# Kernel tuning notes

Measured on AMD Instinct MI355X. Metric: run time of the kernel, lower is better.

The kernel has to match this reference:

```python
import jax, jax.numpy as jnp
import numpy as np

T, N, D, E, L = 3, 50000, 64, 800000, 2


def setup_inputs() -> dict:
    key = jax.random.key(0)
    ks = jax.random.split(key, 12)
    glorot = lambda k, shape: jax.random.uniform(
        k, shape, jnp.float32, -1.0, 1.0) * np.sqrt(6.0 / (shape[-2] + shape[-1]))
    return {
        "x": jax.random.normal(ks[0], (N, D), jnp.float32),
        "edge_index": jax.random.randint(ks[1], (2, E), 0, N),
        "edge_type": jax.random.randint(ks[2], (E,), 0, T),
        "edge_feature": jax.random.normal(ks[3], (T, D), jnp.float32),
        # per-layer parameters stacked along leading L axis
        "theta_g": glorot(ks[4], (L, T, D)),
        "theta_hi": glorot(ks[5], (L, T, D)),
        "theta_hj": glorot(ks[6], (L, T, D)),
        "we": glorot(ks[7], (L, D, D)),
        "wr": glorot(ks[8], (L, D, D)),
    }


def _scatter_softmax(r, row, n):
    # r: [T,E], softmax over edges grouped by destination node `row`
    rT = r.T  # [E,T]
    m = jax.ops.segment_max(rT, row, num_segments=n)  # [N,T]
    e = jnp.exp(rT - m[row])
    s = jax.ops.segment_sum(e, row, num_segments=n)
    return (e / s[row]).T  # [T,E]


def _layer(x, ef, tg, thi, thj, we, wr, row, col, etype, n):
    # attention logits per edge, per type-slice
    r_g = jnp.einsum('ed,td->te', ef, tg)[:, etype]          # [T,E]
    r_hi = jnp.einsum('tnd,td->tn', x, thi)[:, row]          # [T,E]
    r_hj = jnp.einsum('tnd,td->tn', x, thj)[:, col]          # [T,E]
    r = _scatter_softmax(r_g + r_hi + r_hj, row, n)          # [T,E]
    ef_new = ef @ wr                                         # [et,D]
    v = jax.nn.sigmoid(ef_new)[etype][None] * (x @ we)[:, col]  # [T,E,D]
    out = r[..., None] * v                                   # [T,E,D]
    out = jax.ops.segment_sum(out.transpose(1, 0, 2), row, num_segments=n)
    return out.transpose(1, 0, 2), ef_new                    # [T,N,D]


def reference(x, edge_index, edge_type, edge_feature, theta_g, theta_hi, theta_hj, we, wr):
    row, col = edge_index[0], edge_index[1]
    h = jnp.broadcast_to(x[None], (T, N, D))
    ef = edge_feature
    for i in range(L):
        h_prev = h
        out, ef = _layer(h, ef, theta_g[i], theta_hi[i], theta_hj[i],
                         we[i], wr[i], row, col, edge_type, N)
        if i == L - 1:
            h = out
            break
        h = h_prev + jax.nn.relu(out)  # dropout p=0 -> identity
        ef = jax.nn.relu(ef)
    return h
```

## Files before the change

kernel.cpp:

```cpp
#include <hip/hip_runtime.h>
#include <math.h>

#define TT 3
#define NN 50000
#define DD 64
#define EE 800000
#define LL 2
#define NK3 (NN * TT)
#define NB3 ((NK3 + 255) / 256)
#define CH 96

typedef _Float16 h4 __attribute__((ext_vector_type(4)));
typedef float f4 __attribute__((ext_vector_type(4)));

__global__ void k_small(const float* __restrict__ ef0,
                        const float* __restrict__ tg,
                        const float* __restrict__ wr,
                        const float* __restrict__ we,
                        const float* __restrict__ thj,
                        float* __restrict__ rg,
                        float* __restrict__ sig,
                        _Float16* __restrict__ bf)
{
    __shared__ float ef_l[TT * DD];
    __shared__ float efn[TT * DD];
    int tid = threadIdx.x;
    for (int l = 0; l < LL; ++l)
        for (int idx = tid; idx < 80 * 64; idx += 256) {
            int c = idx >> 6, k = idx & 63;
            float v = 0.f;
            if (c < 64) v = we[l * 4096 + k * 64 + c];
            else if (c < 67) v = thj[l * 192 + (c - 64) * 64 + k];
            bf[l * 5120 + idx] = (_Float16)v;
        }
    if (tid < TT * DD) ef_l[tid] = ef0[tid];
    __syncthreads();
    for (int layer = 0; layer < LL; ++layer) {
        if (tid < TT * TT) {
            int t = tid / TT, tau = tid % TT;
            float s = 0.f;
            #pragma unroll
            for (int k = 0; k < DD; ++k)
                s += ef_l[tau * DD + k] * tg[layer * TT * DD + t * DD + k];
            rg[layer * TT * TT + tid] = s;
        }
        if (tid < TT * DD) {
            int tau = tid / DD, d = tid % DD;
            float s = 0.f;
            #pragma unroll
            for (int k = 0; k < DD; ++k)
                s += ef_l[tau * DD + k] * wr[layer * DD * DD + k * DD + d];
            efn[tid] = s;
            sig[layer * TT * DD + tid] = 1.f / (1.f + expf(-s));
        }
        __syncthreads();
        if (tid < TT * DD) ef_l[tid] = fmaxf(efn[tid], 0.f);
        __syncthreads();
    }
}

__global__ void k_count3r(const int* __restrict__ row, const int* __restrict__ et,
                          int* __restrict__ counts, unsigned* __restrict__ keyrank)
{
    int e = blockIdx.x * 256 + threadIdx.x;
    if (e < EE) {
        int key = row[e] * 3 + et[e];
        int r = atomicAdd(&counts[key], 1);
        keyrank[e] = ((unsigned)key << 14) | (unsigned)r;
    }
}

__global__ void k_bsum(const int* __restrict__ counts, int* __restrict__ bsum)
{
    __shared__ int red[256];
    int i = blockIdx.x * 256 + threadIdx.x;
    red[threadIdx.x] = (i < NK3) ? counts[i] : 0;
    __syncthreads();
    for (int off = 128; off >= 1; off >>= 1) {
        if (threadIdx.x < off) red[threadIdx.x] += red[threadIdx.x + off];
        __syncthreads();
    }
    if (threadIdx.x == 0) bsum[blockIdx.x] = red[0];
}

__global__ void k_emit2(const int* __restrict__ counts,
                        const int* __restrict__ bsum,
                        int* __restrict__ csroff)
{
    __shared__ int s[256];
    __shared__ int bpre_s;
    int b = blockIdx.x, tid = threadIdx.x;
    int pp = 0;
    for (int i = tid; i < b; i += 256) pp += bsum[i];
    s[tid] = pp;
    __syncthreads();
    for (int off = 128; off >= 1; off >>= 1) {
        if (tid < off) s[tid] += s[tid + off];
        __syncthreads();
    }
    if (tid == 0) bpre_s = s[0];
    __syncthreads();
    int bpre = bpre_s;
    int idx = b * 256 + tid;
    int c = (idx < NK3) ? counts[idx] : 0;
    s[tid] = c;
    __syncthreads();
    for (int off = 1; off < 256; off <<= 1) {
        int u = (tid >= off) ? s[tid - off] : 0;
        __syncthreads();
        s[tid] += u;
        __syncthreads();
    }
    if (idx < NK3) csroff[idx] = bpre + s[tid] - c;
    if (b == NB3 - 1 && tid == 255) csroff[NK3] = bpre + s[255];
}

__global__ void k_scatter3r(const unsigned* __restrict__ keyrank,
                            const int* __restrict__ col,
                            const int* __restrict__ csroff,
                            unsigned short* __restrict__ pk)
{
    int e = blockIdx.x * 256 + threadIdx.x;
    if (e < EE) {
        unsigned kr = keyrank[e];
        int pos = csroff[kr >> 14] + (int)(kr & 16383u);
        pk[pos] = (unsigned short)col[e];
    }
}

__global__ __launch_bounds__(256) void k_mm0(
    const float* __restrict__ x,
    const _Float16* __restrict__ Bf,
    _Float16* __restrict__ hw,
    float* __restrict__ ahj)
{
    __shared__ _Float16 Ah[64][68];
    __shared__ _Float16 Bt[80][68];
    int tid = threadIdx.x;
    long rbase = (long)blockIdx.x * 64;

    #pragma unroll
    for (int it = 0; it < 4; ++it) {
        int flat = (tid + it * 256) * 4;
        int r = flat >> 6, k = flat & 63;
        h4 hv = {};
        if (rbase + r < NN) {
            float4 v = *(const float4*)&x[(rbase + r) * 64 + k];
            hv = h4{ (_Float16)v.x, (_Float16)v.y, (_Float16)v.z, (_Float16)v.w };
        }
        *(h4*)&Ah[r][k] = hv;
    }
    for (int e4 = tid; e4 < 80 * 64 / 4; e4 += 256) {
        int idx = e4 * 4;
        *(h4*)&Bt[idx >> 6][idx & 63] = *(const h4*)&Bf[idx];
    }
    __syncthreads();

    int wid = tid >> 6, lane = tid & 63;
    int r16 = lane & 15, kq = lane >> 4;
    f4 acc[5] = {};
    #pragma unroll
    for (int ks = 0; ks < 4; ++ks) {
        int k0 = ks * 16 + kq * 4;
        h4 a = *(h4*)&Ah[wid * 16 + r16][k0];
        #pragma unroll
        for (int ct = 0; ct < 5; ++ct) {
            h4 b = *(h4*)&Bt[ct * 16 + r16][k0];
            acc[ct] = __builtin_amdgcn_mfma_f32_16x16x16f16(a, b, acc[ct], 0, 0, 0);
        }
    }
    #pragma unroll
    for (int j = 0; j < 4; ++j) {
        long g = rbase + wid * 16 + kq * 4 + j;
        if (g < NN) {
            #pragma unroll
            for (int ct = 0; ct < 4; ++ct)
                hw[g * 64 + ct * 16 + r16] = (_Float16)acc[ct][j];
            if (r16 < 3) ahj[g * 4 + r16] = acc[4][j];
        }
    }
}

__global__ __launch_bounds__(256) void k_mm1(
    const _Float16* __restrict__ h,
    const _Float16* __restrict__ Bf,
    _Float16* __restrict__ hw,
    float* __restrict__ ahj)
{
    __shared__ _Float16 Ah[64][68];
    __shared__ _Float16 Bt[80][68];
    int tid = threadIdx.x;
    long rbase = (long)blockIdx.x * 64;

    #pragma unroll
    for (int it = 0; it < 4; ++it) {
        int flat = (tid + it * 256) * 4;
        int r = flat >> 6, k = flat & 63;
        h4 hv = {};
        if (rbase + r < NK3) hv = *(const h4*)&h[(rbase + r) * 64 + k];
        *(h4*)&Ah[r][k] = hv;
    }
    for (int e4 = tid; e4 < 80 * 64 / 4; e4 += 256) {
        int idx = e4 * 4;
        *(h4*)&Bt[idx >> 6][idx & 63] = *(const h4*)&Bf[idx];
    }
    __syncthreads();

    int wid = tid >> 6, lane = tid & 63;
    int r16 = lane & 15, kq = lane >> 4;
    f4 acc[5] = {};
    #pragma unroll
    for (int ks = 0; ks < 4; ++ks) {
        int k0 = ks * 16 + kq * 4;
        h4 a = *(h4*)&Ah[wid * 16 + r16][k0];
        #pragma unroll
        for (int ct = 0; ct < 5; ++ct) {
            h4 b = *(h4*)&Bt[ct * 16 + r16][k0];
            acc[ct] = __builtin_amdgcn_mfma_f32_16x16x16f16(a, b, acc[ct], 0, 0, 0);
        }
    }
    #pragma unroll
    for (int j = 0; j < 4; ++j) {
        long g = rbase + wid * 16 + kq * 4 + j;
        if (g < NK3) {
            int t = (g >= 2L * NN) ? 2 : (g >= NN ? 1 : 0);
            long n = g - (long)t * NN;
            #pragma unroll
            for (int ct = 0; ct < 4; ++ct)
                hw[((size_t)n * 3 + t) * 64 + ct * 16 + r16] = (_Float16)acc[ct][j];
            if (r16 == t) ahj[n * 4 + t] = acc[4][j];
        }
    }
}

__global__ __launch_bounds__(256) void k_edge0(
    const int* __restrict__ off3,
    const unsigned short* __restrict__ pk,
    const float* __restrict__ rg_l,
    const float* __restrict__ sig_l,
    const float* __restrict__ ahj4,
    const _Float16* __restrict__ hw,
    const float* __restrict__ x,
    _Float16* __restrict__ outh)
{
    __shared__ uint4 ent[4][CH];
    int wid = threadIdx.x >> 6, lane = threadIdx.x & 63;
    int n = blockIdx.x * 4 + wid;
    int b3 = n * 3;
    int s0 = off3[b3], s1 = off3[b3 + 1], s2 = off3[b3 + 2], s3 = off3[b3 + 3];
    float r00 = rg_l[0], r01 = rg_l[1], r02 = rg_l[2];
    float r10 = rg_l[3], r11 = rg_l[4], r12 = rg_l[5];
    float r20 = rg_l[6], r21 = rg_l[7], r22 = rg_l[8];
    float sg0 = sig_l[lane], sg1 = sig_l[64 + lane], sg2 = sig_l[128 + lane];
    const char* hwb = (const char*)hw + (size_t)lane * 2;
    uint4* myent = ent[wid];
    float acc0 = 0.f, acc1 = 0.f, acc2 = 0.f;
    float ps0 = 0.f, ps1 = 0.f, ps2 = 0.f;

    for (int base = s0; base < s3; base += CH) {
        int cnt = s3 - base; if (cnt > CH) cnt = CH;
        for (int jj = lane; jj < cnt; jj += 64) {
            int ei = base + jj;
            int c = pk[ei];
            int tau = (ei >= s1) + (ei >= s2);
            float4 aj = *(const float4*)&ahj4[c * 4];
            float g0 = (tau == 0) ? r00 : ((tau == 1) ? r01 : r02);
            float g1 = (tau == 0) ? r10 : ((tau == 1) ? r11 : r12);
            float g2 = (tau == 0) ? r20 : ((tau == 1) ? r21 : r22);
            float p0 = __expf(g0 + aj.x);
            float p1 = __expf(g1 + aj.y);
            float p2 = __expf(g2 + aj.z);
            ps0 += p0; ps1 += p1; ps2 += p2;
            myent[jj] = make_uint4(((unsigned)c * 128u) | ((unsigned)tau << 26),
                                   __float_as_uint(p0), __float_as_uint(p1),
                                   __float_as_uint(p2));
        }
        asm volatile("s_waitcnt lgkmcnt(0)" ::: "memory");

#define AGG(J) { uint4 e = myent[J];                                           \
        unsigned ta = e.x >> 26;                                               \
        float sg = (ta == 0) ? sg0 : ((ta == 1) ? sg1 : sg2);                  \
        float sv = sg * (float)*(const _Float16*)(hwb + (e.x & 0x03FFFFFFu));  \
        acc0 = fmaf(__uint_as_float(e.y), sv, acc0);                           \
        acc1 = fmaf(__uint_as_float(e.z), sv, acc1);                           \
        acc2 = fmaf(__uint_as_float(e.w), sv, acc2); }
        int j = 0;
        for (; j + 4 <= cnt; j += 4) { AGG(j) AGG(j + 1) AGG(j + 2) AGG(j + 3) }
        for (; j < cnt; ++j) { AGG(j) }
#undef AGG
        asm volatile("s_waitcnt lgkmcnt(0)" ::: "memory");
    }
    #pragma unroll
    for (int off = 32; off >= 1; off >>= 1) {
        ps0 += __shfl_xor(ps0, off);
        ps1 += __shfl_xor(ps1, off);
        ps2 += __shfl_xor(ps2, off);
    }
    float o0 = 0.f, o1 = 0.f, o2 = 0.f;
    if (s3 > s0) { o0 = acc0 / ps0; o1 = acc1 / ps1; o2 = acc2 / ps2; }
    size_t oi = (size_t)n * 64 + lane;
    float xv = x[oi];
    outh[oi]                       = (_Float16)(xv + fmaxf(o0, 0.f));
    outh[oi + (size_t)NN * 64]     = (_Float16)(xv + fmaxf(o1, 0.f));
    outh[oi + (size_t)2 * NN * 64] = (_Float16)(xv + fmaxf(o2, 0.f));
}

__global__ __launch_bounds__(256) void k_edge1(
    const int* __restrict__ off3,
    const unsigned short* __restrict__ pk,
    const float* __restrict__ rg_l,
    const float* __restrict__ sig_l,
    const float* __restrict__ ahj4,
    const _Float16* __restrict__ hw,
    float* __restrict__ outf)
{
    __shared__ uint4 ent[4][CH];
    int wid = threadIdx.x >> 6, lane = threadIdx.x & 63;
    int n = blockIdx.x * 4 + wid;
    int b3 = n * 3;
    int s0 = off3[b3], s1 = off3[b3 + 1], s2 = off3[b3 + 2], s3 = off3[b3 + 3];
    float r00 = rg_l[0], r01 = rg_l[1], r02 = rg_l[2];
    float r10 = rg_l[3], r11 = rg_l[4], r12 = rg_l[5];
    float r20 = rg_l[6], r21 = rg_l[7], r22 = rg_l[8];
    float sg0 = sig_l[lane], sg1 = sig_l[64 + lane], sg2 = sig_l[128 + lane];
    const char* hwb = (const char*)hw + (size_t)lane * 2;
    uint4* myent = ent[wid];
    float acc0 = 0.f, acc1 = 0.f, acc2 = 0.f;
    float ps0 = 0.f, ps1 = 0.f, ps2 = 0.f;

    for (int base = s0; base < s3; base += CH) {
        int cnt = s3 - base; if (cnt > CH) cnt = CH;
        for (int jj = lane; jj < cnt; jj += 64) {
            int ei = base + jj;
            int c = pk[ei];
            int tau = (ei >= s1) + (ei >= s2);
            float4 aj = *(const float4*)&ahj4[c * 4];
            float g0 = (tau == 0) ? r00 : ((tau == 1) ? r01 : r02);
            float g1 = (tau == 0) ? r10 : ((tau == 1) ? r11 : r12);
            float g2 = (tau == 0) ? r20 : ((tau == 1) ? r21 : r22);
            float p0 = __expf(g0 + aj.x);
            float p1 = __expf(g1 + aj.y);
            float p2 = __expf(g2 + aj.z);
            ps0 += p0; ps1 += p1; ps2 += p2;
            myent[jj] = make_uint4(((unsigned)c * 384u) | ((unsigned)tau << 26),
                                   __float_as_uint(p0), __float_as_uint(p1),
                                   __float_as_uint(p2));
        }
        asm volatile("s_waitcnt lgkmcnt(0)" ::: "memory");

#define AGG(J) { uint4 e = myent[J];                                           \
        unsigned ta = e.x >> 26;                                               \
        float sg = (ta == 0) ? sg0 : ((ta == 1) ? sg1 : sg2);                  \
        const char* ptr = hwb + (e.x & 0x03FFFFFFu);                           \
        float v0 = (float)*(const _Float16*)(ptr);                             \
        float v1 = (float)*(const _Float16*)(ptr + 128);                       \
        float v2 = (float)*(const _Float16*)(ptr + 256);                       \
        acc0 = fmaf(__uint_as_float(e.y), sg * v0, acc0);                      \
        acc1 = fmaf(__uint_as_float(e.z), sg * v1, acc1);                      \
        acc2 = fmaf(__uint_as_float(e.w), sg * v2, acc2); }
        int j = 0;
        for (; j + 4 <= cnt; j += 4) { AGG(j) AGG(j + 1) AGG(j + 2) AGG(j + 3) }
        for (; j < cnt; ++j) { AGG(j) }
#undef AGG
        asm volatile("s_waitcnt lgkmcnt(0)" ::: "memory");
    }
    #pragma unroll
    for (int off = 32; off >= 1; off >>= 1) {
        ps0 += __shfl_xor(ps0, off);
        ps1 += __shfl_xor(ps1, off);
        ps2 += __shfl_xor(ps2, off);
    }
    float o0 = 0.f, o1 = 0.f, o2 = 0.f;
    if (s3 > s0) { o0 = acc0 / ps0; o1 = acc1 / ps1; o2 = acc2 / ps2; }
    size_t oi = (size_t)n * 64 + lane;
    outf[oi]                       = o0;
    outf[oi + (size_t)NN * 64]     = o1;
    outf[oi + (size_t)2 * NN * 64] = o2;
}

extern "C" void kernel_launch(void* const* d_in, const int* in_sizes, int n_in,
                              void* d_out, int out_size, void* d_ws, size_t ws_size,
                              hipStream_t stream)
{
    const float* x   = (const float*)d_in[0];
    const int*   ei  = (const int*)d_in[1];
    const int*   row = ei;
    const int*   col = ei + EE;
    const int*   et  = (const int*)d_in[2];
    const float* ef  = (const float*)d_in[3];
    const float* tg  = (const float*)d_in[4];
    const float* thj = (const float*)d_in[6];
    const float* we  = (const float*)d_in[7];
    const float* wr  = (const float*)d_in[8];
    float* out = (float*)d_out;
    _Float16* h1h = (_Float16*)d_out;

    _Float16* hw1 = (_Float16*)d_ws;
    _Float16* hw0 = hw1 + (size_t)NN * 3 * 64;
    float* ahj0 = (float*)(hw0 + (size_t)NN * 64);
    float* ahj1 = ahj0 + (size_t)NN * 4;
    float* rg   = ahj1 + (size_t)NN * 4;
    float* sig  = rg + LL * 9;
    _Float16* bfB = (_Float16*)(sig + LL * 192);
    int* counts3 = (int*)(bfB + LL * 5120);
    int* csroff3 = counts3 + NK3;
    int* bsum    = csroff3 + NK3 + 1;
    unsigned* keyrank = (unsigned*)(bsum + NB3);
    unsigned short* csrpk = (unsigned short*)(keyrank + EE);

    hipMemsetAsync(counts3, 0, NK3 * sizeof(int), stream);
    k_small<<<1, 256, 0, stream>>>(ef, tg, wr, we, thj, rg, sig, bfB);
    k_count3r<<<(EE + 255) / 256, 256, 0, stream>>>(row, et, counts3, keyrank);
    k_bsum<<<NB3, 256, 0, stream>>>(counts3, bsum);
    k_emit2<<<NB3, 256, 0, stream>>>(counts3, bsum, csroff3);
    k_scatter3r<<<(EE + 255) / 256, 256, 0, stream>>>(keyrank, col, csroff3, csrpk);

    k_mm0<<<(NN + 63) / 64, 256, 0, stream>>>(x, bfB, hw0, ahj0);
    k_edge0<<<NN / 4, 256, 0, stream>>>(csroff3, csrpk, rg, sig, ahj0, hw0,
                                        x, h1h);
    k_mm1<<<(NK3 + 63) / 64, 256, 0, stream>>>(h1h, bfB + 5120, hw1, ahj1);
    k_edge1<<<NN / 4, 256, 0, stream>>>(csroff3, csrpk, rg + 9, sig + 192,
                                        ahj1, hw1, out);
}
```

Baseline: 179.5 us.

## Fuse count, layer-0 matmul and small setup into one kernel; fuse layer-1 matmul into edge0

Merges the edge counting, the first-layer feature matmul and the tiny parameter-setup kernel into one launch that dispatches by block index, so independent work shares a grid. The layer-1 matmul is folded into the end of the layer-0 edge kernel: per-node results are staged in shared memory and multiplied with MFMA instead of being written to global memory and read back. It also adds an 8-way unroll in the layer-1 aggregation loop. In exchange, the fused matmul uses only 3 of 16 MFMA rows, each edge block must load the weight tile and sync, and the extra shared memory may lower occupancy.

```diff
diff --git a/kernel.cpp b/kernel.cpp
--- a/kernel.cpp
+++ b/kernel.cpp
@@ -9,22 +9,88 @@
 #define NK3 (NN * TT)
 #define NB3 ((NK3 + 255) / 256)
 #define CH 96
+#define NBC ((EE + 255) / 256)
+#define NBM ((NN + 63) / 64)
 
 typedef _Float16 h4 __attribute__((ext_vector_type(4)));
 typedef float f4 __attribute__((ext_vector_type(4)));
 
-__global__ void k_small(const float* __restrict__ ef0,
-                        const float* __restrict__ tg,
-                        const float* __restrict__ wr,
-                        const float* __restrict__ we,
-                        const float* __restrict__ thj,
-                        float* __restrict__ rg,
-                        float* __restrict__ sig,
-                        _Float16* __restrict__ bf)
-{
-    __shared__ float ef_l[TT * DD];
-    __shared__ float efn[TT * DD];
-    int tid = threadIdx.x;
+__global__ __launch_bounds__(256) void k_fusedA(
+    const int* __restrict__ row, const int* __restrict__ et,
+    int* __restrict__ counts, unsigned* __restrict__ keyrank,
+    const float* __restrict__ x,
+    const float* __restrict__ we,
+    const float* __restrict__ thj,
+    _Float16* __restrict__ hw0,
+    float* __restrict__ ahj0,
+    const float* __restrict__ ef0,
+    const float* __restrict__ tg,
+    const float* __restrict__ wr,
+    float* __restrict__ rg,
+    float* __restrict__ sig,
+    _Float16* __restrict__ bf)
+{
+    __shared__ _Float16 Ah[64][68];
+    __shared__ _Float16 Bt[80][68];
+    int b = blockIdx.x, tid = threadIdx.x;
+
+    if (b < NBC) {
+        int e = b * 256 + tid;
+        if (e < EE) {
+            int key = row[e] * 3 + et[e];
+            int r = atomicAdd(&counts[key], 1);
+            keyrank[e] = ((unsigned)key << 14) | (unsigned)r;
+        }
+        return;
+    }
+    if (b < NBC + NBM) {
+        long rbase = (long)(b - NBC) * 64;
+        #pragma unroll
+        for (int it = 0; it < 4; ++it) {
+            int flat = (tid + it * 256) * 4;
+            int r = flat >> 6, k = flat & 63;
+            h4 hv = {};
+            if (rbase + r < NN) {
+                float4 v = *(const float4*)&x[(rbase + r) * 64 + k];
+                hv = h4{ (_Float16)v.x, (_Float16)v.y, (_Float16)v.z, (_Float16)v.w };
+            }
+            *(h4*)&Ah[r][k] = hv;
+        }
+        for (int idx = tid; idx < 80 * 64; idx += 256) {
+            int c = idx >> 6, k = idx & 63;
+            float v = 0.f;
+            if (c < 64) v = we[k * 64 + c];
+            else if (c < 67) v = thj[(c - 64) * 64 + k];
+            Bt[c][k] = (_Float16)v;
+        }
+        __syncthreads();
+        int wid = tid >> 6, lane = tid & 63;
+        int r16 = lane & 15, kq = lane >> 4;
+        f4 acc[5] = {};
+        #pragma unroll
+        for (int ks = 0; ks < 4; ++ks) {
+            int k0 = ks * 16 + kq * 4;
+            h4 a = *(h4*)&Ah[wid * 16 + r16][k0];
+            #pragma unroll
+            for (int ct = 0; ct < 5; ++ct) {
+                h4 bb = *(h4*)&Bt[ct * 16 + r16][k0];
+                acc[ct] = __builtin_amdgcn_mfma_f32_16x16x16f16(a, bb, acc[ct], 0, 0, 0);
+            }
+        }
+        #pragma unroll
+        for (int j = 0; j < 4; ++j) {
+            long g = rbase + wid * 16 + kq * 4 + j;
+            if (g < NN) {
+                #pragma unroll
+                for (int ct = 0; ct < 4; ++ct)
+                    hw0[g * 64 + ct * 16 + r16] = (_Float16)acc[ct][j];
+                if (r16 < 3) ahj0[g * 4 + r16] = acc[4][j];
+            }
+        }
+        return;
+    }
+    float* ef_l = (float*)&Ah[0][0];
+    float* efn  = ef_l + TT * DD;
     for (int l = 0; l < LL; ++l)
         for (int idx = tid; idx < 80 * 64; idx += 256) {
             int c = idx >> 6, k = idx & 63;
@@ -59,17 +125,6 @@
     }
 }
 
-__global__ void k_count3r(const int* __restrict__ row, const int* __restrict__ et,
-                          int* __restrict__ counts, unsigned* __restrict__ keyrank)
-{
-    int e = blockIdx.x * 256 + threadIdx.x;
-    if (e < EE) {
-        int key = row[e] * 3 + et[e];
-        int r = atomicAdd(&counts[key], 1);
-        keyrank[e] = ((unsigned)key << 14) | (unsigned)r;
-    }
-}
-
 __global__ void k_bsum(const int* __restrict__ counts, int* __restrict__ bsum)
 {
     __shared__ int red[256];
@@ -128,112 +183,7 @@
     }
 }
 
-__global__ __launch_bounds__(256) void k_mm0(
-    const float* __restrict__ x,
-    const _Float16* __restrict__ Bf,
-    _Float16* __restrict__ hw,
-    float* __restrict__ ahj)
-{
-    __shared__ _Float16 Ah[64][68];
-    __shared__ _Float16 Bt[80][68];
-    int tid = threadIdx.x;
-    long rbase = (long)blockIdx.x * 64;
-
-    #pragma unroll
-    for (int it = 0; it < 4; ++it) {
-        int flat = (tid + it * 256) * 4;
-        int r = flat >> 6, k = flat & 63;
-        h4 hv = {};
-        if (rbase + r < NN) {
-            float4 v = *(const float4*)&x[(rbase + r) * 64 + k];
-            hv = h4{ (_Float16)v.x, (_Float16)v.y, (_Float16)v.z, (_Float16)v.w };
-        }
-        *(h4*)&Ah[r][k] = hv;
-    }
-    for (int e4 = tid; e4 < 80 * 64 / 4; e4 += 256) {
-        int idx = e4 * 4;
-        *(h4*)&Bt[idx >> 6][idx & 63] = *(const h4*)&Bf[idx];
-    }
-    __syncthreads();
-
-    int wid = tid >> 6, lane = tid & 63;
-    int r16 = lane & 15, kq = lane >> 4;
-    f4 acc[5] = {};
-    #pragma unroll
-    for (int ks = 0; ks < 4; ++ks) {
-        int k0 = ks * 16 + kq * 4;
-        h4 a = *(h4*)&Ah[wid * 16 + r16][k0];
-        #pragma unroll
-        for (int ct = 0; ct < 5; ++ct) {
-            h4 b = *(h4*)&Bt[ct * 16 + r16][k0];
-            acc[ct] = __builtin_amdgcn_mfma_f32_16x16x16f16(a, b, acc[ct], 0, 0, 0);
-        }
-    }
-    #pragma unroll
-    for (int j = 0; j < 4; ++j) {
-        long g = rbase + wid * 16 + kq * 4 + j;
-        if (g < NN) {
-            #pragma unroll
-            for (int ct = 0; ct < 4; ++ct)
-                hw[g * 64 + ct * 16 + r16] = (_Float16)acc[ct][j];
-            if (r16 < 3) ahj[g * 4 + r16] = acc[4][j];
-        }
-    }
-}
-
-__global__ __launch_bounds__(256) void k_mm1(
-    const _Float16* __restrict__ h,
-    const _Float16* __restrict__ Bf,
-    _Float16* __restrict__ hw,
-    float* __restrict__ ahj)
-{
-    __shared__ _Float16 Ah[64][68];
-    __shared__ _Float16 Bt[80][68];
-    int tid = threadIdx.x;
-    long rbase = (long)blockIdx.x * 64;
-
-    #pragma unroll
-    for (int it = 0; it < 4; ++it) {
-        int flat = (tid + it * 256) * 4;
-        int r = flat >> 6, k = flat & 63;
-        h4 hv = {};
-        if (rbase + r < NK3) hv = *(const h4*)&h[(rbase + r) * 64 + k];
-        *(h4*)&Ah[r][k] = hv;
-    }
-    for (int e4 = tid; e4 < 80 * 64 / 4; e4 += 256) {
-        int idx = e4 * 4;
-        *(h4*)&Bt[idx >> 6][idx & 63] = *(const h4*)&Bf[idx];
-    }
-    __syncthreads();
-
-    int wid = tid >> 6, lane = tid & 63;
-    int r16 = lane & 15, kq = lane >> 4;
-    f4 acc[5] = {};
-    #pragma unroll
-    for (int ks = 0; ks < 4; ++ks) {
-        int k0 = ks * 16 + kq * 4;
-        h4 a = *(h4*)&Ah[wid * 16 + r16][k0];
-        #pragma unroll
-        for (int ct = 0; ct < 5; ++ct) {
-            h4 b = *(h4*)&Bt[ct * 16 + r16][k0];
-            acc[ct] = __builtin_amdgcn_mfma_f32_16x16x16f16(a, b, acc[ct], 0, 0, 0);
-        }
-    }
-    #pragma unroll
-    for (int j = 0; j < 4; ++j) {
-        long g = rbase + wid * 16 + kq * 4 + j;
-        if (g < NK3) {
-            int t = (g >= 2L * NN) ? 2 : (g >= NN ? 1 : 0);
-            long n = g - (long)t * NN;
-            #pragma unroll
-            for (int ct = 0; ct < 4; ++ct)
-                hw[((size_t)n * 3 + t) * 64 + ct * 16 + r16] = (_Float16)acc[ct][j];
-            if (r16 == t) ahj[n * 4 + t] = acc[4][j];
-        }
-    }
-}
-
-__global__ __launch_bounds__(256) void k_edge0(
+__global__ __launch_bounds__(256) void k_edge0mm(
     const int* __restrict__ off3,
     const unsigned short* __restrict__ pk,
     const float* __restrict__ rg_l,
@@ -241,11 +191,21 @@
     const float* __restrict__ ahj4,
     const _Float16* __restrict__ hw,
     const float* __restrict__ x,
-    _Float16* __restrict__ outh)
+    const _Float16* __restrict__ Bf1,
+    _Float16* __restrict__ hw1,
+    float* __restrict__ ahj1)
 {
     __shared__ uint4 ent[4][CH];
-    int wid = threadIdx.x >> 6, lane = threadIdx.x & 63;
+    __shared__ _Float16 Bt[80][68];
+    __shared__ _Float16 As[4][3][68];
+    int tid = threadIdx.x, wid = tid >> 6, lane = tid & 63;
     int n = blockIdx.x * 4 + wid;
+
+    for (int e4 = tid; e4 < 80 * 64 / 4; e4 += 256) {
+        int idx = e4 * 4;
+        *(h4*)&Bt[idx >> 6][idx & 63] = *(const h4*)&Bf1[idx];
+    }
+
     int b3 = n * 3;
     int s0 = off3[b3], s1 = off3[b3 + 1], s2 = off3[b3 + 2], s3 = off3[b3 + 3];
     float r00 = rg_l[0], r01 = rg_l[1], r02 = rg_l[2];
@@ -298,11 +258,37 @@
     }
     float o0 = 0.f, o1 = 0.f, o2 = 0.f;
     if (s3 > s0) { o0 = acc0 / ps0; o1 = acc1 / ps1; o2 = acc2 / ps2; }
-    size_t oi = (size_t)n * 64 + lane;
-    float xv = x[oi];
-    outh[oi]                       = (_Float16)(xv + fmaxf(o0, 0.f));
-    outh[oi + (size_t)NN * 64]     = (_Float16)(xv + fmaxf(o1, 0.f));
-    outh[oi + (size_t)2 * NN * 64] = (_Float16)(xv + fmaxf(o2, 0.f));
+    float xv = x[(size_t)n * 64 + lane];
+    As[wid][0][lane] = (_Float16)(xv + fmaxf(o0, 0.f));
+    As[wid][1][lane] = (_Float16)(xv + fmaxf(o1, 0.f));
+    As[wid][2][lane] = (_Float16)(xv + fmaxf(o2, 0.f));
+    __syncthreads();
+
+    int r16 = lane & 15, kq = lane >> 4;
+    int ar = (r16 < 3) ? r16 : 0;
+    f4 acc[5] = {};
+    #pragma unroll
+    for (int ks = 0; ks < 4; ++ks) {
+        int k0 = ks * 16 + kq * 4;
+        h4 a = *(h4*)&As[wid][ar][k0];
+        #pragma unroll
+        for (int ct = 0; ct < 5; ++ct) {
+            h4 bb = *(h4*)&Bt[ct * 16 + r16][k0];
+            acc[ct] = __builtin_amdgcn_mfma_f32_16x16x16f16(a, bb, acc[ct], 0, 0, 0);
+        }
+    }
+    if (kq == 0) {
+        #pragma unroll
+        for (int ct = 0; ct < 4; ++ct) {
+            hw1[((size_t)n * 3 + 0) * 64 + ct * 16 + r16] = (_Float16)acc[ct][0];
+            hw1[((size_t)n * 3 + 1) * 64 + ct * 16 + r16] = (_Float16)acc[ct][1];
+            hw1[((size_t)n * 3 + 2) * 64 + ct * 16 + r16] = (_Float16)acc[ct][2];
+        }
+        if (r16 < 3) {
+            float av = (r16 == 0) ? acc[4][0] : ((r16 == 1) ? acc[4][1] : acc[4][2]);
+            ahj1[n * 4 + r16] = av;
+        }
+    }
 }
 
 __global__ __launch_bounds__(256) void k_edge1(
@@ -359,6 +345,8 @@
         acc1 = fmaf(__uint_as_float(e.z), sg * v1, acc1);                      \
         acc2 = fmaf(__uint_as_float(e.w), sg * v2, acc2); }
         int j = 0;
+        for (; j + 8 <= cnt; j += 8) { AGG(j) AGG(j + 1) AGG(j + 2) AGG(j + 3)
+                                       AGG(j + 4) AGG(j + 5) AGG(j + 6) AGG(j + 7) }
         for (; j + 4 <= cnt; j += 4) { AGG(j) AGG(j + 1) AGG(j + 2) AGG(j + 3) }
         for (; j < cnt; ++j) { AGG(j) }
 #undef AGG
@@ -393,7 +381,6 @@
     const float* we  = (const float*)d_in[7];
     const float* wr  = (const float*)d_in[8];
     float* out = (float*)d_out;
-    _Float16* h1h = (_Float16*)d_out;
 
     _Float16* hw1 = (_Float16*)d_ws;
     _Float16* hw0 = hw1 + (size_t)NN * 3 * 64;
@@ -409,16 +396,14 @@
     unsigned short* csrpk = (unsigned short*)(keyrank + EE);
 
     hipMemsetAsync(counts3, 0, NK3 * sizeof(int), stream);
-    k_small<<<1, 256, 0, stream>>>(ef, tg, wr, we, thj, rg, sig, bfB);
-    k_count3r<<<(EE + 255) / 256, 256, 0, stream>>>(row, et, counts3, keyrank);
+    k_fusedA<<<NBC + NBM + 1, 256, 0, stream>>>(row, et, counts3, keyrank,
+                                                x, we, thj, hw0, ahj0,
+                                                ef, tg, wr, rg, sig, bfB);
     k_bsum<<<NB3, 256, 0, stream>>>(counts3, bsum);
     k_emit2<<<NB3, 256, 0, stream>>>(counts3, bsum, csroff3);
     k_scatter3r<<<(EE + 255) / 256, 256, 0, stream>>>(keyrank, col, csroff3, csrpk);
-
-    k_mm0<<<(NN + 63) / 64, 256, 0, stream>>>(x, bfB, hw0, ahj0);
-    k_edge0<<<NN / 4, 256, 0, stream>>>(csroff3, csrpk, rg, sig, ahj0, hw0,
-                                        x, h1h);
-    k_mm1<<<(NK3 + 63) / 64, 256, 0, stream>>>(h1h, bfB + 5120, hw1, ahj1);
+    k_edge0mm<<<NN / 4, 256, 0, stream>>>(csroff3, csrpk, rg, sig, ahj0, hw0,
+                                          x, bfB + 5120, hw1, ahj1);
     k_edge1<<<NN / 4, 256, 0, stream>>>(csroff3, csrpk, rg + 9, sig + 192,
                                         ahj1, hw1, out);
 }
```

Measured after the change: 204.1 us. +13.7%, slower.

## Merge edge counting, layer-0 matmul and small setup into one kernel

Applied to the files above, without the earlier changes.

Launches a single kernel whose block ranges do different jobs: edge key counting with atomics, the layer-0 x@we/thj MFMA matmul (building fp16 weights in shared memory directly from fp32 inputs instead of reading a precomputed buffer), and the small edge-feature setup in the last block. This removes two launches and lets independent work run concurrently instead of being serialized by stream order. It also adds an 8-way unrolled aggregation loop in both edge kernels to expose more memory-level parallelism, at some cost in register pressure.

```diff
diff --git a/kernel.cpp b/kernel.cpp
--- a/kernel.cpp
+++ b/kernel.cpp
@@ -9,22 +9,88 @@
 #define NK3 (NN * TT)
 #define NB3 ((NK3 + 255) / 256)
 #define CH 96
+#define NBC ((EE + 255) / 256)
+#define NBM ((NN + 63) / 64)
 
 typedef _Float16 h4 __attribute__((ext_vector_type(4)));
 typedef float f4 __attribute__((ext_vector_type(4)));
 
-__global__ void k_small(const float* __restrict__ ef0,
-                        const float* __restrict__ tg,
-                        const float* __restrict__ wr,
-                        const float* __restrict__ we,
-                        const float* __restrict__ thj,
-                        float* __restrict__ rg,
-                        float* __restrict__ sig,
-                        _Float16* __restrict__ bf)
-{
-    __shared__ float ef_l[TT * DD];
-    __shared__ float efn[TT * DD];
-    int tid = threadIdx.x;
+__global__ __launch_bounds__(256) void k_fusedA(
+    const int* __restrict__ row, const int* __restrict__ et,
+    int* __restrict__ counts, unsigned* __restrict__ keyrank,
+    const float* __restrict__ x,
+    const float* __restrict__ we,
+    const float* __restrict__ thj,
+    _Float16* __restrict__ hw0,
+    float* __restrict__ ahj0,
+    const float* __restrict__ ef0,
+    const float* __restrict__ tg,
+    const float* __restrict__ wr,
+    float* __restrict__ rg,
+    float* __restrict__ sig,
+    _Float16* __restrict__ bf)
+{
+    __shared__ _Float16 Ah[64][68];
+    __shared__ _Float16 Bt[80][68];
+    int b = blockIdx.x, tid = threadIdx.x;
+
+    if (b < NBC) {
+        int e = b * 256 + tid;
+        if (e < EE) {
+            int key = row[e] * 3 + et[e];
+            int r = atomicAdd(&counts[key], 1);
+            keyrank[e] = ((unsigned)key << 14) | (unsigned)r;
+        }
+        return;
+    }
+    if (b < NBC + NBM) {
+        long rbase = (long)(b - NBC) * 64;
+        #pragma unroll
+        for (int it = 0; it < 4; ++it) {
+            int flat = (tid + it * 256) * 4;
+            int r = flat >> 6, k = flat & 63;
+            h4 hv = {};
+            if (rbase + r < NN) {
+                float4 v = *(const float4*)&x[(rbase + r) * 64 + k];
+                hv = h4{ (_Float16)v.x, (_Float16)v.y, (_Float16)v.z, (_Float16)v.w };
+            }
+            *(h4*)&Ah[r][k] = hv;
+        }
+        for (int idx = tid; idx < 80 * 64; idx += 256) {
+            int c = idx >> 6, k = idx & 63;
+            float v = 0.f;
+            if (c < 64) v = we[k * 64 + c];
+            else if (c < 67) v = thj[(c - 64) * 64 + k];
+            Bt[c][k] = (_Float16)v;
+        }
+        __syncthreads();
+        int wid = tid >> 6, lane = tid & 63;
+        int r16 = lane & 15, kq = lane >> 4;
+        f4 acc[5] = {};
+        #pragma unroll
+        for (int ks = 0; ks < 4; ++ks) {
+            int k0 = ks * 16 + kq * 4;
+            h4 a = *(h4*)&Ah[wid * 16 + r16][k0];
+            #pragma unroll
+            for (int ct = 0; ct < 5; ++ct) {
+                h4 bb = *(h4*)&Bt[ct * 16 + r16][k0];
+                acc[ct] = __builtin_amdgcn_mfma_f32_16x16x16f16(a, bb, acc[ct], 0, 0, 0);
+            }
+        }
+        #pragma unroll
+        for (int j = 0; j < 4; ++j) {
+            long g = rbase + wid * 16 + kq * 4 + j;
+            if (g < NN) {
+                #pragma unroll
+                for (int ct = 0; ct < 4; ++ct)
+                    hw0[g * 64 + ct * 16 + r16] = (_Float16)acc[ct][j];
+                if (r16 < 3) ahj0[g * 4 + r16] = acc[4][j];
+            }
+        }
+        return;
+    }
+    float* ef_l = (float*)&Ah[0][0];
+    float* efn  = ef_l + TT * DD;
     for (int l = 0; l < LL; ++l)
         for (int idx = tid; idx < 80 * 64; idx += 256) {
             int c = idx >> 6, k = idx & 63;
@@ -59,17 +125,6 @@
     }
 }
 
-__global__ void k_count3r(const int* __restrict__ row, const int* __restrict__ et,
-                          int* __restrict__ counts, unsigned* __restrict__ keyrank)
-{
-    int e = blockIdx.x * 256 + threadIdx.x;
-    if (e < EE) {
-        int key = row[e] * 3 + et[e];
-        int r = atomicAdd(&counts[key], 1);
-        keyrank[e] = ((unsigned)key << 14) | (unsigned)r;
-    }
-}
-
 __global__ void k_bsum(const int* __restrict__ counts, int* __restrict__ bsum)
 {
     __shared__ int red[256];
@@ -125,59 +180,6 @@
         unsigned kr = keyrank[e];
         int pos = csroff[kr >> 14] + (int)(kr & 16383u);
         pk[pos] = (unsigned short)col[e];
-    }
-}
-
-__global__ __launch_bounds__(256) void k_mm0(
-    const float* __restrict__ x,
-    const _Float16* __restrict__ Bf,
-    _Float16* __restrict__ hw,
-    float* __restrict__ ahj)
-{
-    __shared__ _Float16 Ah[64][68];
-    __shared__ _Float16 Bt[80][68];
-    int tid = threadIdx.x;
-    long rbase = (long)blockIdx.x * 64;
-
-    #pragma unroll
-    for (int it = 0; it < 4; ++it) {
-        int flat = (tid + it * 256) * 4;
-        int r = flat >> 6, k = flat & 63;
-        h4 hv = {};
-        if (rbase + r < NN) {
-            float4 v = *(const float4*)&x[(rbase + r) * 64 + k];
-            hv = h4{ (_Float16)v.x, (_Float16)v.y, (_Float16)v.z, (_Float16)v.w };
-        }
-        *(h4*)&Ah[r][k] = hv;
-    }
-    for (int e4 = tid; e4 < 80 * 64 / 4; e4 += 256) {
-        int idx = e4 * 4;
-        *(h4*)&Bt[idx >> 6][idx & 63] = *(const h4*)&Bf[idx];
-    }
-    __syncthreads();
-
-    int wid = tid >> 6, lane = tid & 63;
-    int r16 = lane & 15, kq = lane >> 4;
-    f4 acc[5] = {};
-    #pragma unroll
-    for (int ks = 0; ks < 4; ++ks) {
-        int k0 = ks * 16 + kq * 4;
-        h4 a = *(h4*)&Ah[wid * 16 + r16][k0];
-        #pragma unroll
-        for (int ct = 0; ct < 5; ++ct) {
-            h4 b = *(h4*)&Bt[ct * 16 + r16][k0];
-            acc[ct] = __builtin_amdgcn_mfma_f32_16x16x16f16(a, b, acc[ct], 0, 0, 0);
-        }
-    }
-    #pragma unroll
-    for (int j = 0; j < 4; ++j) {
-        long g = rbase + wid * 16 + kq * 4 + j;
-        if (g < NN) {
-            #pragma unroll
-            for (int ct = 0; ct < 4; ++ct)
-                hw[g * 64 + ct * 16 + r16] = (_Float16)acc[ct][j];
-            if (r16 < 3) ahj[g * 4 + r16] = acc[4][j];
-        }
     }
 }
 
@@ -285,6 +287,8 @@
         acc1 = fmaf(__uint_as_float(e.z), sv, acc1);                           \
         acc2 = fmaf(__uint_as_float(e.w), sv, acc2); }
         int j = 0;
+        for (; j + 8 <= cnt; j += 8) { AGG(j) AGG(j + 1) AGG(j + 2) AGG(j + 3)
+                                       AGG(j + 4) AGG(j + 5) AGG(j + 6) AGG(j + 7) }
         for (; j + 4 <= cnt; j += 4) { AGG(j) AGG(j + 1) AGG(j + 2) AGG(j + 3) }
         for (; j < cnt; ++j) { AGG(j) }
 #undef AGG
@@ -359,6 +363,8 @@
         acc1 = fmaf(__uint_as_float(e.z), sg * v1, acc1);                      \
         acc2 = fmaf(__uint_as_float(e.w), sg * v2, acc2); }
         int j = 0;
+        for (; j + 8 <= cnt; j += 8) { AGG(j) AGG(j + 1) AGG(j + 2) AGG(j + 3)
+                                       AGG(j + 4) AGG(j + 5) AGG(j + 6) AGG(j + 7) }
         for (; j + 4 <= cnt; j += 4) { AGG(j) AGG(j + 1) AGG(j + 2) AGG(j + 3) }
         for (; j < cnt; ++j) { AGG(j) }
 #undef AGG
@@ -409,13 +415,12 @@
     unsigned short* csrpk = (unsigned short*)(keyrank + EE);
 
     hipMemsetAsync(counts3, 0, NK3 * sizeof(int), stream);
-    k_small<<<1, 256, 0, stream>>>(ef, tg, wr, we, thj, rg, sig, bfB);
-    k_count3r<<<(EE + 255) / 256, 256, 0, stream>>>(row, et, counts3, keyrank);
+    k_fusedA<<<NBC + NBM + 1, 256, 0, stream>>>(row, et, counts3, keyrank,
+                                                x, we, thj, hw0, ahj0,
+                                                ef, tg, wr, rg, sig, bfB);
     k_bsum<<<NB3, 256, 0, stream>>>(counts3, bsum);
     k_emit2<<<NB3, 256, 0, stream>>>(counts3, bsum, csroff3);
     k_scatter3r<<<(EE + 255) / 256, 256, 0, stream>>>(keyrank, col, csroff3, csrpk);
-
-    k_mm0<<<(NN + 63) / 64, 256, 0, stream>>>(x, bfB, hw0, ahj0);
     k_edge0<<<NN / 4, 256, 0, stream>>>(csroff3, csrpk, rg, sig, ahj0, hw0,
                                         x, h1h);
     k_mm1<<<(NK3 + 63) / 64, 256, 0, stream>>>(h1h, bfB + 5120, hw1, ahj1);
```

Result: no change. 179.4 us (-0.1%).
